# Optimization experiments

Hardware: AMD Instinct MI355X
Metric: run time of the kernel (lower is better)

The kernel has to match this reference:

```python
import jax, jax.numpy as jnp
import numpy as np

FP16_HUGE = 2.0 ** 15
NUM_HEAD = 4
LN_EPS = 1e-5


def setup_inputs() -> dict:
    key = jax.random.key(0)
    ks = jax.random.split(key, 12)
    B, N, D = 1, 256, 128
    H = NUM_HEAD
    inp = {
        "pair_act": jax.random.normal(ks[0], (B, N, N, D), dtype=jnp.float32),
        "pair_mask": jnp.ones((B, N, N), dtype=jnp.float32),
        "ln_scale": jnp.ones((D,), dtype=jnp.float32),
        "ln_bias": jnp.zeros((D,), dtype=jnp.float32),
        # torch Linear weight layout: [out_dim, in_dim]; applied as x @ W.T
        "w2d": jax.random.normal(ks[1], (H, D), dtype=jnp.float32) / np.sqrt(D),
        "wq": jax.random.normal(ks[2], (D, D), dtype=jnp.float32) / np.sqrt(D),
        "wk": jax.random.normal(ks[3], (D, D), dtype=jnp.float32) / np.sqrt(D),
        "wv": jax.random.normal(ks[4], (D, D), dtype=jnp.float32) / np.sqrt(D),
        "wg": jax.random.normal(ks[5], (D, D), dtype=jnp.float32) / np.sqrt(D),
        "bg": jnp.ones((D,), dtype=jnp.float32),  # gating bias init = 1.0
        "wo": jax.random.normal(ks[6], (D, D), dtype=jnp.float32) * 0.02,
        "bo": jnp.zeros((D,), dtype=jnp.float32),
    }
    return inp


def reference(pair_act, pair_mask, ln_scale, ln_bias, w2d, wq, wk, wv, wg, bg, wo, bo):
    B, N, _, D = pair_act.shape
    H = NUM_HEAD
    kd = D // H  # per-head key/value dim
    scale = kd ** (-0.5)

    # mask bias: [B, N(row), 1, 1, N(key)]
    bias = (FP16_HUGE * (pair_mask - 1.0))[:, :, None, None, :]

    # LayerNorm (fp32, eps=1e-5)
    mu = jnp.mean(pair_act, axis=-1, keepdims=True)
    var = jnp.mean(jnp.square(pair_act - mu), axis=-1, keepdims=True)
    x = (pair_act - mu) * jax.lax.rsqrt(var + LN_EPS) * ln_scale + ln_bias

    # non-batched per-head bias: [B, 1, H, N, N]
    nb = jnp.einsum("bijd,hd->bhij", x, w2d)[:, None]

    q = (x @ wq.T).reshape(B, N, N, H, kd) * scale  # [B, r, i, H, kd]
    k = (x @ wk.T).reshape(B, N, N, H, kd)
    v = (x @ wv.T).reshape(B, N, N, H, kd)

    logits = jnp.einsum("brihk,brjhk->brhij", q, k) + bias + nb  # [B, r, H, i, j]
    w = jax.nn.softmax(logits, axis=-1)
    o = jnp.einsum("brhij,brjhv->brihv", w, v)  # [B, r, i, H, kd]

    g = jax.nn.sigmoid(x @ wg.T + bg).reshape(B, N, N, H, kd)
    o = (o * g).reshape(B, N, N, D)

    out = o @ wo.T + bo
    return out * pair_mask[..., None]
```

## Files before the change

### kernel.cpp

```cpp
#include <hip/hip_runtime.h>
#include <hip/hip_bf16.h>

typedef unsigned short u16;
typedef __attribute__((ext_vector_type(8))) short bf16x8;
typedef __attribute__((ext_vector_type(4))) float f32x4;
typedef __attribute__((address_space(3))) unsigned lds_u32;
typedef const __attribute__((address_space(1))) unsigned glb_u32;

#define N 256
#define D 128
#define NH 4
#define KD 32
#define NN 65536
#define QK_SCALE 0.17677669529663687f
#define LOG2E 1.4426950408889634f
#define HUGE_MASK 32768.0f

__device__ __forceinline__ float b2f(u16 s) {
  union { float f; unsigned u; } x; x.u = ((unsigned)s) << 16; return x.f;
}
__device__ __forceinline__ u16 f2b(float f) {
  union { float f; unsigned u; } x; x.f = f;
  unsigned r = x.u + 0x7fff + ((x.u >> 16) & 1);
  return (u16)(r >> 16);
}
__device__ __forceinline__ float exp2v(float x) {
  float r; __asm__("v_exp_f32 %0, %1" : "=v"(r) : "v"(x)); return r;
}

__global__ __launch_bounds__(256) void prep_w_kernel(
    const float* __restrict__ wq, const float* __restrict__ wk,
    const float* __restrict__ wv, const float* __restrict__ wg,
    const float* __restrict__ wo, u16* __restrict__ wb)
{
  int idx = blockIdx.x * 256 + threadIdx.x;
  const float* srcs[5] = {wq, wk, wv, wg, wo};
  int mat = idx >> 11, rem = idx & 2047;
  int row = rem >> 4, g = rem & 15;
  int gp = (g + (row & 15)) & 15;
  const float* s = srcs[mat] + row * 128 + g * 8;
  float4 f0 = *(const float4*)(s);
  float4 f1 = *(const float4*)(s + 4);
  uint4 pk;
  pk.x = (unsigned)f2b(f0.x) | ((unsigned)f2b(f0.y) << 16);
  pk.y = (unsigned)f2b(f0.z) | ((unsigned)f2b(f0.w) << 16);
  pk.z = (unsigned)f2b(f1.x) | ((unsigned)f2b(f1.y) << 16);
  pk.w = (unsigned)f2b(f1.z) | ((unsigned)f2b(f1.w) << 16);
  *(uint4*)(wb + (size_t)mat * 16384 + row * 128 + gp * 8) = pk;
}

template <int NW>
__device__ __forceinline__ void async_stage(const u16* __restrict__ gsrc, u16* lds, int tid) {
  int lane = tid & 63, wave = tid >> 6;
#pragma unroll
  for (int p = 0; p < 32 / NW; p++) {
    int c = wave * (32 / NW) + p;
    __builtin_amdgcn_global_load_lds((glb_u32*)(gsrc + c * 512 + lane * 8),
                                     (lds_u32*)(lds + c * 512), 16, 0, 0);
  }
}

__global__ __launch_bounds__(512) void projln_kernel(
    const float* __restrict__ pa, const float* __restrict__ lns, const float* __restrict__ lnb,
    const float* __restrict__ w2d, const u16* __restrict__ wb, const float* __restrict__ bg,
    u16* __restrict__ q, u16* __restrict__ k, u16* __restrict__ v, u16* __restrict__ g,
    float* __restrict__ nb)
{
  __shared__ __align__(16) u16 Wl[2][16384];
  int tid = threadIdx.x;
  int wave = tid >> 6, lane = tid & 63;
  int lr = lane & 15, quad = lane >> 4;

  async_stage<8>(wb, Wl[0], tid);

  bf16x8 a[4];
  int row = blockIdx.x * 128 + wave * 16 + lr;
  {
    const float* rp = pa + (size_t)row * D;
    float xv[4][8];
    float s = 0.f, ss = 0.f;
#pragma unroll
    for (int ks = 0; ks < 4; ks++) {
      float4 a0 = *(const float4*)(rp + ks * 32 + quad * 8);
      float4 a1 = *(const float4*)(rp + ks * 32 + quad * 8 + 4);
      xv[ks][0] = a0.x; xv[ks][1] = a0.y; xv[ks][2] = a0.z; xv[ks][3] = a0.w;
      xv[ks][4] = a1.x; xv[ks][5] = a1.y; xv[ks][6] = a1.z; xv[ks][7] = a1.w;
#pragma unroll
      for (int j = 0; j < 8; j++) { s += xv[ks][j]; ss += xv[ks][j] * xv[ks][j]; }
    }
    s  += __shfl_xor(s, 16, 64);  ss += __shfl_xor(ss, 16, 64);
    s  += __shfl_xor(s, 32, 64);  ss += __shfl_xor(ss, 32, 64);
    float mu = s * (1.0f / D);
    float var = ss * (1.0f / D) - mu * mu;
    float rs = rsqrtf(var + 1e-5f);
#pragma unroll
    for (int ks = 0; ks < 4; ks++) {
      float4 s0 = *(const float4*)(lns + ks * 32 + quad * 8);
      float4 s1 = *(const float4*)(lns + ks * 32 + quad * 8 + 4);
      float4 b0 = *(const float4*)(lnb + ks * 32 + quad * 8);
      float4 b1 = *(const float4*)(lnb + ks * 32 + quad * 8 + 4);
      float sc[8] = {s0.x,s0.y,s0.z,s0.w,s1.x,s1.y,s1.z,s1.w};
      float bi[8] = {b0.x,b0.y,b0.z,b0.w,b1.x,b1.y,b1.z,b1.w};
#pragma unroll
      for (int j = 0; j < 8; j++) xv[ks][j] = (xv[ks][j] - mu) * rs * sc[j] + bi[j];
    }
#pragma unroll
    for (int h = 0; h < NH; h++) {
      float p = 0.f;
#pragma unroll
      for (int ks = 0; ks < 4; ks++) {
        float4 w0 = *(const float4*)(w2d + h * D + ks * 32 + quad * 8);
        float4 w1 = *(const float4*)(w2d + h * D + ks * 32 + quad * 8 + 4);
        p += xv[ks][0]*w0.x + xv[ks][1]*w0.y + xv[ks][2]*w0.z + xv[ks][3]*w0.w
           + xv[ks][4]*w1.x + xv[ks][5]*w1.y + xv[ks][6]*w1.z + xv[ks][7]*w1.w;
      }
      p += __shfl_xor(p, 16, 64);
      p += __shfl_xor(p, 32, 64);
      if (quad == 0)
        nb[(size_t)h * NN + row] = p * LOG2E;
    }
#pragma unroll
    for (int ks = 0; ks < 4; ks++)
#pragma unroll
      for (int j = 0; j < 8; j++) a[ks][j] = (short)f2b(xv[ks][j]);
  }
  __syncthreads();

  u16* Os[4] = {q, k, v, g};
#pragma unroll
  for (int mat = 0; mat < 4; mat++) {
    if (mat < 3) async_stage<8>(wb + (size_t)(mat + 1) * 16384, Wl[(mat + 1) & 1], tid);
    const u16* Wcur = Wl[mat & 1];
    f32x4 acc[2][4];
#pragma unroll
    for (int tg = 0; tg < 2; tg++)
#pragma unroll
      for (int e = 0; e < 4; e++) acc[tg][e] = (f32x4){0.f, 0.f, 0.f, 0.f};
#pragma unroll
    for (int ks = 0; ks < 4; ks++) {
#pragma unroll
      for (int tg = 0; tg < 2; tg++) {
#pragma unroll
        for (int e = 0; e < 4; e++) {
          int nrow = tg * 64 + 4 * lr + e;
          int gp = (ks * 4 + quad + (nrow & 15)) & 15;
          bf16x8 b = *(const bf16x8*)(&Wcur[nrow * 128 + gp * 8]);
          acc[tg][e] = __builtin_amdgcn_mfma_f32_16x16x32_bf16(a[ks], b, acc[tg][e], 0, 0, 0);
        }
      }
    }
    u16* O = Os[mat];
    int row0 = blockIdx.x * 128 + wave * 16 + quad * 4;
#pragma unroll
    for (int tg = 0; tg < 2; tg++) {
      int c0 = tg * 64 + 4 * lr;
      float bg0 = 0.f, bg1 = 0.f, bg2 = 0.f, bg3 = 0.f;
      if (mat == 3) { bg0 = bg[c0]; bg1 = bg[c0+1]; bg2 = bg[c0+2]; bg3 = bg[c0+3]; }
#pragma unroll
      for (int reg = 0; reg < 4; reg++) {
        float v0 = acc[tg][0][reg], v1 = acc[tg][1][reg];
        float v2 = acc[tg][2][reg], v3 = acc[tg][3][reg];
        if (mat == 0) {
          v0 *= QK_SCALE * LOG2E; v1 *= QK_SCALE * LOG2E;
          v2 *= QK_SCALE * LOG2E; v3 *= QK_SCALE * LOG2E;
        }
        if (mat == 3) {
          v0 = 1.0f / (1.0f + __expf(-(v0 + bg0)));
          v1 = 1.0f / (1.0f + __expf(-(v1 + bg1)));
          v2 = 1.0f / (1.0f + __expf(-(v2 + bg2)));
          v3 = 1.0f / (1.0f + __expf(-(v3 + bg3)));
        }
        uint2 pk;
        pk.x = (unsigned)f2b(v0) | ((unsigned)f2b(v1) << 16);
        pk.y = (unsigned)f2b(v2) | ((unsigned)f2b(v3) << 16);
        *(uint2*)(O + (size_t)(row0 + reg) * D + c0) = pk;
      }
    }
    __syncthreads();
  }
}

__global__ __launch_bounds__(512) void attn_kernel(
    const u16* __restrict__ q, const u16* __restrict__ k, const u16* __restrict__ v,
    const u16* __restrict__ g, const float* __restrict__ nb, const float* __restrict__ mask,
    u16* __restrict__ og)
{
  __shared__ __align__(16) u16 Kf[8192];
  __shared__ __align__(16) u16 Vf[8192];
  __shared__ float bias_lds[256];
  int h = blockIdx.x & 3, r = blockIdx.x >> 2;
  int tid = threadIdx.x;
  {
    int j = tid & 255;
    if (tid < 256) {
      const u16* krow = k + ((size_t)r * N + j) * D + h * KD;
      int t = j >> 4, lrj = j & 15;
#pragma unroll
      for (int qc = 0; qc < 4; qc++)
        *(bf16x8*)(&Kf[((t * 4 + qc) * 16 + lrj) * 8]) = *(const bf16x8*)(krow + qc * 8);
      bias_lds[j] = (HUGE_MASK * LOG2E) * (mask[r * N + j] - 1.0f);
    }
    const u16* vrow = v + ((size_t)r * N + j) * D + h * KD;
    int ksrc = j >> 5, jrel = j & 31;
    int qv, jv;
    if (jrel < 16) { qv = jrel >> 2; jv = jrel & 3; }
    else           { qv = (jrel & 15) >> 2; jv = 4 + (jrel & 3); }
    int chalf = (tid >> 8) * 16;
#pragma unroll
    for (int cc = 0; cc < 16; cc++) {
      int c = chalf + cc;
      Vf[(((ksrc * 2 + (c & 1)) * 4 + qv) * 16 + (c >> 1)) * 8 + jv] = vrow[c];
    }
  }
  __syncthreads();
  int wave = tid >> 6, lane = tid & 63;
  int lr = lane & 15, quad = lane >> 4;
  const float* nbh = nb + (size_t)h * NN;

  for (int pp = 0; pp < 2; pp++) {
    int i0 = pp * 128 + wave * 16;
    int irow = i0 + lr;
    bf16x8 af = *(const bf16x8*)(q + ((size_t)r * N + irow) * D + h * KD + quad * 8);
    const float* nbrow = nbh + (size_t)irow * N;
    float m = 0.f, ls = 0.f;
    f32x4 oa = (f32x4){0.f,0.f,0.f,0.f}, ob = (f32x4){0.f,0.f,0.f,0.f};
#pragma unroll 1
    for (int c = 0; c < 2; c++) {
      f32x4 S[8];
#pragma unroll
      for (int tt = 0; tt < 8; tt++) {
        int t = c * 8 + tt;
        int jb = t * 16 + quad * 4;
        float4 nb4 = *(const float4*)(nbrow + jb);
        float4 b4  = *(const float4*)(&bias_lds[jb]);
        f32x4 ci;
        ci[0] = nb4.x + b4.x; ci[1] = nb4.y + b4.y;
        ci[2] = nb4.z + b4.z; ci[3] = nb4.w + b4.w;
        bf16x8 kfr = *(const bf16x8*)(&Kf[((t * 4 + quad) * 16 + lr) * 8]);
        S[tt] = __builtin_amdgcn_mfma_f32_16x16x32_bf16(kfr, af, ci, 0, 0, 0);
      }
      float m0 = -3e38f, m1 = -3e38f, m2 = -3e38f, m3 = -3e38f;
#pragma unroll
      for (int tt = 0; tt < 8; tt++) {
        m0 = fmaxf(m0, S[tt][0]); m1 = fmaxf(m1, S[tt][1]);
        m2 = fmaxf(m2, S[tt][2]); m3 = fmaxf(m3, S[tt][3]);
      }
      float ma = fmaxf(fmaxf(m0, m1), fmaxf(m2, m3));
      ma = fmaxf(ma, __shfl_xor(ma, 16, 64));
      ma = fmaxf(ma, __shfl_xor(ma, 32, 64));
      if (c == 0) {
        m = ma;
      } else {
        float mnew = fmaxf(m, ma);
        float sc = exp2v(m - mnew);
        m = mnew;
        ls *= sc;
        float s0 = __shfl(sc, quad * 4 + 0, 64);
        float s1 = __shfl(sc, quad * 4 + 1, 64);
        float s2 = __shfl(sc, quad * 4 + 2, 64);
        float s3 = __shfl(sc, quad * 4 + 3, 64);
        oa[0] *= s0; oa[1] *= s1; oa[2] *= s2; oa[3] *= s3;
        ob[0] *= s0; ob[1] *= s1; ob[2] *= s2; ob[3] *= s3;
      }
#pragma unroll
      for (int kk = 0; kk < 4; kk++) {
        int ks = c * 4 + kk;
        float p0 = exp2v(S[2*kk][0] - m);
        float p1 = exp2v(S[2*kk][1] - m);
        float p2 = exp2v(S[2*kk][2] - m);
        float p3 = exp2v(S[2*kk][3] - m);
        float p4 = exp2v(S[2*kk+1][0] - m);
        float p5 = exp2v(S[2*kk+1][1] - m);
        float p6 = exp2v(S[2*kk+1][2] - m);
        float p7 = exp2v(S[2*kk+1][3] - m);
        ls += ((p0 + p1) + (p2 + p3)) + ((p4 + p5) + (p6 + p7));
        union { bf16x8 v; unsigned u[4]; } pa;
        __asm__("v_cvt_pk_bf16_f32 %0, %1, %2" : "=v"(pa.u[0]) : "v"(p0), "v"(p1));
        __asm__("v_cvt_pk_bf16_f32 %0, %1, %2" : "=v"(pa.u[1]) : "v"(p2), "v"(p3));
        __asm__("v_cvt_pk_bf16_f32 %0, %1, %2" : "=v"(pa.u[2]) : "v"(p4), "v"(p5));
        __asm__("v_cvt_pk_bf16_f32 %0, %1, %2" : "=v"(pa.u[3]) : "v"(p6), "v"(p7));
        bf16x8 vb0 = *(const bf16x8*)(&Vf[(((ks * 2 + 0) * 4 + quad) * 16 + lr) * 8]);
        oa = __builtin_amdgcn_mfma_f32_16x16x32_bf16(pa.v, vb0, oa, 0, 0, 0);
        bf16x8 vb1 = *(const bf16x8*)(&Vf[(((ks * 2 + 1) * 4 + quad) * 16 + lr) * 8]);
        ob = __builtin_amdgcn_mfma_f32_16x16x32_bf16(pa.v, vb1, ob, 0, 0, 0);
      }
    }
    float lsum = ls;
    lsum += __shfl_xor(lsum, 16, 64);
    lsum += __shfl_xor(lsum, 32, 64);
    float invd = __builtin_amdgcn_rcpf(lsum);

#pragma unroll
    for (int reg = 0; reg < 4; reg++) {
      float inv = __shfl(invd, quad * 4 + reg, 64);
      int i = i0 + quad * 4 + reg;
      size_t base = ((size_t)r * N + i) * D + h * KD + 2 * lr;
      unsigned gv = *(const unsigned*)(g + base);
      float r0 = oa[reg] * inv * b2f((u16)(gv & 0xffff));
      float r1 = ob[reg] * inv * b2f((u16)(gv >> 16));
      *(unsigned*)(og + base) = (unsigned)f2b(r0) | ((unsigned)f2b(r1) << 16);
    }
  }
}

__global__ __launch_bounds__(512) void out_kernel(
    const u16* __restrict__ og, const u16* __restrict__ wob, const float* __restrict__ bo,
    const float* __restrict__ mask, float* __restrict__ out)
{
  __shared__ __align__(16) u16 Wlds[16384];
  int tid = threadIdx.x;
  async_stage<8>(wob, Wlds, tid);
  int wave = tid >> 6, lane = tid & 63;
  int lr = lane & 15, quad = lane >> 4;
  bf16x8 a[4];
  int arow = blockIdx.x * 128 + wave * 16 + lr;
#pragma unroll
  for (int ks = 0; ks < 4; ks++)
    a[ks] = *(const bf16x8*)(og + (size_t)arow * D + ks * 32 + quad * 8);
  __syncthreads();
  f32x4 acc[2][4];
#pragma unroll
  for (int tg = 0; tg < 2; tg++)
#pragma unroll
    for (int e = 0; e < 4; e++) acc[tg][e] = (f32x4){0.f, 0.f, 0.f, 0.f};
#pragma unroll
  for (int ks = 0; ks < 4; ks++) {
#pragma unroll
    for (int tg = 0; tg < 2; tg++) {
#pragma unroll
      for (int e = 0; e < 4; e++) {
        int nrow = tg * 64 + 4 * lr + e;
        int gp = (ks * 4 + quad + (nrow & 15)) & 15;
        bf16x8 b = *(const bf16x8*)(&Wlds[nrow * 128 + gp * 8]);
        acc[tg][e] = __builtin_amdgcn_mfma_f32_16x16x32_bf16(a[ks], b, acc[tg][e], 0, 0, 0);
      }
    }
  }
  int row0 = blockIdx.x * 128 + wave * 16 + quad * 4;
#pragma unroll
  for (int tg = 0; tg < 2; tg++) {
    int c0 = tg * 64 + 4 * lr;
    float4 bo4 = *(const float4*)(bo + c0);
#pragma unroll
    for (int reg = 0; reg < 4; reg++) {
      int pos = row0 + reg;
      float mk = mask[pos];
      float4 o4;
      o4.x = (acc[tg][0][reg] + bo4.x) * mk;
      o4.y = (acc[tg][1][reg] + bo4.y) * mk;
      o4.z = (acc[tg][2][reg] + bo4.z) * mk;
      o4.w = (acc[tg][3][reg] + bo4.w) * mk;
      *(float4*)(out + (size_t)pos * D + c0) = o4;
    }
  }
}

extern "C" void kernel_launch(void* const* d_in, const int* in_sizes, int n_in,
                              void* d_out, int out_size, void* d_ws, size_t ws_size,
                              hipStream_t stream)
{
  const float* pa   = (const float*)d_in[0];
  const float* mask = (const float*)d_in[1];
  const float* lns  = (const float*)d_in[2];
  const float* lnb  = (const float*)d_in[3];
  const float* w2d  = (const float*)d_in[4];
  const float* wq   = (const float*)d_in[5];
  const float* wk   = (const float*)d_in[6];
  const float* wv   = (const float*)d_in[7];
  const float* wg   = (const float*)d_in[8];
  const float* bg   = (const float*)d_in[9];
  const float* wo   = (const float*)d_in[10];
  const float* bo   = (const float*)d_in[11];

  const size_t ARR = (size_t)NN * D;
  u16* q  = (u16*)d_ws;
  u16* k  = q + ARR;
  u16* v  = k + ARR;
  u16* g  = v + ARR;
  u16* og = g + ARR;
  float* nb = (float*)(og + ARR);
  u16* wb = (u16*)(nb + (size_t)NH * NN);

  prep_w_kernel<<<40, 256, 0, stream>>>(wq, wk, wv, wg, wo, wb);
  projln_kernel<<<512, 512, 0, stream>>>(pa, lns, lnb, w2d, wb, bg, q, k, v, g, nb);
  attn_kernel<<<N * NH, 512, 0, stream>>>(q, k, v, g, nb, mask, og);
  out_kernel<<<512, 512, 0, stream>>>(og, wb + 4 * 16384, bo, mask, (float*)d_out);
}
```

Baseline: 186.6 us.

## Fuse attention and output projection into one kernel with per-block head loop

Merges attn_kernel and out_kernel so each block handles half the query rows of one pair row and loops over all four heads. The gated attention output is written to LDS in a swizzled layout instead of global memory, then multiplied by the staged Wo to produce the final output. This removes the og global round trip and one kernel launch. In exchange, K/V for every head are restaged serially with extra syncs, K/V are loaded twice per row (once per half), and the grid shrinks from 1024 to 512 blocks, giving less parallelism.

```diff
diff --git a/kernel.cpp b/kernel.cpp
--- a/kernel.cpp
+++ b/kernel.cpp
@@ -180,48 +180,51 @@
   }
 }
 
-__global__ __launch_bounds__(512) void attn_kernel(
+__global__ __launch_bounds__(512) void attn_out_kernel(
     const u16* __restrict__ q, const u16* __restrict__ k, const u16* __restrict__ v,
     const u16* __restrict__ g, const float* __restrict__ nb, const float* __restrict__ mask,
-    u16* __restrict__ og)
+    const u16* __restrict__ wob, const float* __restrict__ bo, float* __restrict__ out)
 {
-  __shared__ __align__(16) u16 Kf[8192];
-  __shared__ __align__(16) u16 Vf[8192];
+  __shared__ __align__(16) u16 KV[16384];
+  __shared__ __align__(16) u16 og_lds[16384];
   __shared__ float bias_lds[256];
-  int h = blockIdx.x & 3, r = blockIdx.x >> 2;
+  int r = blockIdx.x >> 1, half = blockIdx.x & 1;
   int tid = threadIdx.x;
-  {
-    int j = tid & 255;
-    if (tid < 256) {
-      const u16* krow = k + ((size_t)r * N + j) * D + h * KD;
-      int t = j >> 4, lrj = j & 15;
-#pragma unroll
-      for (int qc = 0; qc < 4; qc++)
-        *(bf16x8*)(&Kf[((t * 4 + qc) * 16 + lrj) * 8]) = *(const bf16x8*)(krow + qc * 8);
-      bias_lds[j] = (HUGE_MASK * LOG2E) * (mask[r * N + j] - 1.0f);
-    }
-    const u16* vrow = v + ((size_t)r * N + j) * D + h * KD;
-    int ksrc = j >> 5, jrel = j & 31;
-    int qv, jv;
-    if (jrel < 16) { qv = jrel >> 2; jv = jrel & 3; }
-    else           { qv = (jrel & 15) >> 2; jv = 4 + (jrel & 3); }
-    int chalf = (tid >> 8) * 16;
+  int wave = tid >> 6, lane = tid & 63;
+  int lr = lane & 15, quad = lane >> 4;
+
+  if (tid < 256) bias_lds[tid] = (HUGE_MASK * LOG2E) * (mask[r * N + tid] - 1.0f);
+
+  int irow = half * 128 + wave * 16 + lr;
+  const u16* qbase = q + ((size_t)r * N + irow) * D + quad * 8;
+  bf16x8 af[NH];
+#pragma unroll
+  for (int h = 0; h < NH; h++) af[h] = *(const bf16x8*)(qbase + h * KD);
+
+  int kj = tid >> 1, kc = tid & 1;
+  int tK = kj >> 4, lrK = kj & 15;
+  int vj = tid & 255;
+  int jrel = vj & 31, ksrc = vj >> 5;
+  int qv = (jrel & 15) >> 2;
+  int jv = (jrel & 3) | ((jrel >> 4) << 2);
+  int chalf = (tid >> 8) * 16;
+
+#pragma unroll 1
+  for (int h = 0; h < NH; h++) {
+    const u16* krow = k + ((size_t)r * N + kj) * D + h * KD + kc * 16;
+    bf16x8 k0 = *(const bf16x8*)(krow);
+    bf16x8 k1 = *(const bf16x8*)(krow + 8);
+    *(bf16x8*)(&KV[((tK * 4 + kc * 2 + 0) * 16 + lrK) * 8]) = k0;
+    *(bf16x8*)(&KV[((tK * 4 + kc * 2 + 1) * 16 + lrK) * 8]) = k1;
+    const u16* vrow = v + ((size_t)r * N + vj) * D + h * KD;
 #pragma unroll
     for (int cc = 0; cc < 16; cc++) {
       int c = chalf + cc;
-      Vf[(((ksrc * 2 + (c & 1)) * 4 + qv) * 16 + (c >> 1)) * 8 + jv] = vrow[c];
-    }
-  }
-  __syncthreads();
-  int wave = tid >> 6, lane = tid & 63;
-  int lr = lane & 15, quad = lane >> 4;
-  const float* nbh = nb + (size_t)h * NN;
-
-  for (int pp = 0; pp < 2; pp++) {
-    int i0 = pp * 128 + wave * 16;
-    int irow = i0 + lr;
-    bf16x8 af = *(const bf16x8*)(q + ((size_t)r * N + irow) * D + h * KD + quad * 8);
-    const float* nbrow = nbh + (size_t)irow * N;
+      KV[8192 + (((ksrc * 2 + (c & 1)) * 4 + qv) * 16 + (c >> 1)) * 8 + jv] = vrow[c];
+    }
+    __syncthreads();
+
+    const float* nbrow = nb + (size_t)h * NN + (size_t)irow * N;
     float m = 0.f, ls = 0.f;
     f32x4 oa = (f32x4){0.f,0.f,0.f,0.f}, ob = (f32x4){0.f,0.f,0.f,0.f};
 #pragma unroll 1
@@ -236,8 +239,8 @@
         f32x4 ci;
         ci[0] = nb4.x + b4.x; ci[1] = nb4.y + b4.y;
         ci[2] = nb4.z + b4.z; ci[3] = nb4.w + b4.w;
-        bf16x8 kfr = *(const bf16x8*)(&Kf[((t * 4 + quad) * 16 + lr) * 8]);
-        S[tt] = __builtin_amdgcn_mfma_f32_16x16x32_bf16(kfr, af, ci, 0, 0, 0);
+        bf16x8 kfr = *(const bf16x8*)(&KV[((t * 4 + quad) * 16 + lr) * 8]);
+        S[tt] = __builtin_amdgcn_mfma_f32_16x16x32_bf16(kfr, af[h], ci, 0, 0, 0);
       }
       float m0 = -3e38f, m1 = -3e38f, m2 = -3e38f, m3 = -3e38f;
 #pragma unroll
@@ -279,9 +282,9 @@
         __asm__("v_cvt_pk_bf16_f32 %0, %1, %2" : "=v"(pa.u[1]) : "v"(p2), "v"(p3));
         __asm__("v_cvt_pk_bf16_f32 %0, %1, %2" : "=v"(pa.u[2]) : "v"(p4), "v"(p5));
         __asm__("v_cvt_pk_bf16_f32 %0, %1, %2" : "=v"(pa.u[3]) : "v"(p6), "v"(p7));
-        bf16x8 vb0 = *(const bf16x8*)(&Vf[(((ks * 2 + 0) * 4 + quad) * 16 + lr) * 8]);
+        bf16x8 vb0 = *(const bf16x8*)(&KV[8192 + (((ks * 2 + 0) * 4 + quad) * 16 + lr) * 8]);
         oa = __builtin_amdgcn_mfma_f32_16x16x32_bf16(pa.v, vb0, oa, 0, 0, 0);
-        bf16x8 vb1 = *(const bf16x8*)(&Vf[(((ks * 2 + 1) * 4 + quad) * 16 + lr) * 8]);
+        bf16x8 vb1 = *(const bf16x8*)(&KV[8192 + (((ks * 2 + 1) * 4 + quad) * 16 + lr) * 8]);
         ob = __builtin_amdgcn_mfma_f32_16x16x32_bf16(pa.v, vb1, ob, 0, 0, 0);
       }
     }
@@ -293,31 +296,29 @@
 #pragma unroll
     for (int reg = 0; reg < 4; reg++) {
       float inv = __shfl(invd, quad * 4 + reg, 64);
-      int i = i0 + quad * 4 + reg;
-      size_t base = ((size_t)r * N + i) * D + h * KD + 2 * lr;
-      unsigned gv = *(const unsigned*)(g + base);
+      int l = wave * 16 + quad * 4 + reg;
+      size_t gb = ((size_t)r * N + half * 128 + l) * D + h * KD + 2 * lr;
+      unsigned gv = *(const unsigned*)(g + gb);
       float r0 = oa[reg] * inv * b2f((u16)(gv & 0xffff));
       float r1 = ob[reg] * inv * b2f((u16)(gv >> 16));
-      *(unsigned*)(og + base) = (unsigned)f2b(r0) | ((unsigned)f2b(r1) << 16);
-    }
-  }
-}
-
-__global__ __launch_bounds__(512) void out_kernel(
-    const u16* __restrict__ og, const u16* __restrict__ wob, const float* __restrict__ bo,
-    const float* __restrict__ mask, float* __restrict__ out)
-{
-  __shared__ __align__(16) u16 Wlds[16384];
-  int tid = threadIdx.x;
-  async_stage<8>(wob, Wlds, tid);
-  int wave = tid >> 6, lane = tid & 63;
-  int lr = lane & 15, quad = lane >> 4;
+      int col = h * KD + 2 * lr;
+      int gp = ((col >> 3) + l) & 15;
+      *(unsigned*)(&og_lds[l * 128 + gp * 8 + (col & 7)]) =
+          (unsigned)f2b(r0) | ((unsigned)f2b(r1) << 16);
+    }
+    __syncthreads();
+  }
+
+  async_stage<8>(wob, KV, tid);
+  __syncthreads();
+
   bf16x8 a[4];
-  int arow = blockIdx.x * 128 + wave * 16 + lr;
-#pragma unroll
-  for (int ks = 0; ks < 4; ks++)
-    a[ks] = *(const bf16x8*)(og + (size_t)arow * D + ks * 32 + quad * 8);
-  __syncthreads();
+  int l = wave * 16 + lr;
+#pragma unroll
+  for (int ks = 0; ks < 4; ks++) {
+    int gp = (ks * 4 + quad + (l & 15)) & 15;
+    a[ks] = *(const bf16x8*)(&og_lds[l * 128 + gp * 8]);
+  }
   f32x4 acc[2][4];
 #pragma unroll
   for (int tg = 0; tg < 2; tg++)
@@ -331,19 +332,19 @@
       for (int e = 0; e < 4; e++) {
         int nrow = tg * 64 + 4 * lr + e;
         int gp = (ks * 4 + quad + (nrow & 15)) & 15;
-        bf16x8 b = *(const bf16x8*)(&Wlds[nrow * 128 + gp * 8]);
+        bf16x8 b = *(const bf16x8*)(&KV[nrow * 128 + gp * 8]);
         acc[tg][e] = __builtin_amdgcn_mfma_f32_16x16x32_bf16(a[ks], b, acc[tg][e], 0, 0, 0);
       }
     }
   }
-  int row0 = blockIdx.x * 128 + wave * 16 + quad * 4;
+  int flat0 = r * N + half * 128 + wave * 16 + quad * 4;
 #pragma unroll
   for (int tg = 0; tg < 2; tg++) {
     int c0 = tg * 64 + 4 * lr;
     float4 bo4 = *(const float4*)(bo + c0);
 #pragma unroll
     for (int reg = 0; reg < 4; reg++) {
-      int pos = row0 + reg;
+      int pos = flat0 + reg;
       float mk = mask[pos];
       float4 o4;
       o4.x = (acc[tg][0][reg] + bo4.x) * mk;
@@ -377,12 +378,11 @@
   u16* k  = q + ARR;
   u16* v  = k + ARR;
   u16* g  = v + ARR;
-  u16* og = g + ARR;
-  float* nb = (float*)(og + ARR);
+  float* nb = (float*)(g + ARR);
   u16* wb = (u16*)(nb + (size_t)NH * NN);
 
   prep_w_kernel<<<40, 256, 0, stream>>>(wq, wk, wv, wg, wo, wb);
   projln_kernel<<<512, 512, 0, stream>>>(pa, lns, lnb, w2d, wb, bg, q, k, v, g, nb);
-  attn_kernel<<<N * NH, 512, 0, stream>>>(q, k, v, g, nb, mask, og);
-  out_kernel<<<512, 512, 0, stream>>>(og, wb + 4 * 16384, bo, mask, (float*)d_out);
-}
+  attn_out_kernel<<<512, 512, 0, stream>>>(q, k, v, g, nb, mask, wb + 4 * 16384, bo,
+                                           (float*)d_out);
+}
```

After: 225.5 us. 20.9% more time.

## Write K and V in attention fragment layout from projection kernel

Applied to the files above, without the earlier changes.

The projection kernel now writes K and V straight into the per-(row, head) fragment layouts that the attention kernel uses in LDS. Attention then stages K/V with linear async global-to-LDS copies instead of a scattered gather and transpose. This removes the scalar, uncoalesced V transpose from the attention prologue. In exchange, the projection epilogue does scattered 2-byte V stores and strided K stores.

```diff
diff --git a/kernel.cpp b/kernel.cpp
--- a/kernel.cpp
+++ b/kernel.cpp
@@ -49,12 +49,12 @@
   *(uint4*)(wb + (size_t)mat * 16384 + row * 128 + gp * 8) = pk;
 }
 
-template <int NW>
-__device__ __forceinline__ void async_stage(const u16* __restrict__ gsrc, u16* lds, int tid) {
+template <int CPW>
+__device__ __forceinline__ void stage_lin(const u16* __restrict__ gsrc, u16* lds, int tid) {
   int lane = tid & 63, wave = tid >> 6;
 #pragma unroll
-  for (int p = 0; p < 32 / NW; p++) {
-    int c = wave * (32 / NW) + p;
+  for (int p = 0; p < CPW; p++) {
+    int c = wave * CPW + p;
     __builtin_amdgcn_global_load_lds((glb_u32*)(gsrc + c * 512 + lane * 8),
                                      (lds_u32*)(lds + c * 512), 16, 0, 0);
   }
@@ -63,7 +63,7 @@
 __global__ __launch_bounds__(512) void projln_kernel(
     const float* __restrict__ pa, const float* __restrict__ lns, const float* __restrict__ lnb,
     const float* __restrict__ w2d, const u16* __restrict__ wb, const float* __restrict__ bg,
-    u16* __restrict__ q, u16* __restrict__ k, u16* __restrict__ v, u16* __restrict__ g,
+    u16* __restrict__ q, u16* __restrict__ kf, u16* __restrict__ vf, u16* __restrict__ g,
     float* __restrict__ nb)
 {
   __shared__ __align__(16) u16 Wl[2][16384];
@@ -71,7 +71,7 @@
   int wave = tid >> 6, lane = tid & 63;
   int lr = lane & 15, quad = lane >> 4;
 
-  async_stage<8>(wb, Wl[0], tid);
+  stage_lin<4>(wb, Wl[0], tid);
 
   bf16x8 a[4];
   int row = blockIdx.x * 128 + wave * 16 + lr;
@@ -126,10 +126,9 @@
   }
   __syncthreads();
 
-  u16* Os[4] = {q, k, v, g};
 #pragma unroll
   for (int mat = 0; mat < 4; mat++) {
-    if (mat < 3) async_stage<8>(wb + (size_t)(mat + 1) * 16384, Wl[(mat + 1) & 1], tid);
+    if (mat < 3) stage_lin<4>(wb + (size_t)(mat + 1) * 16384, Wl[(mat + 1) & 1], tid);
     const u16* Wcur = Wl[mat & 1];
     f32x4 acc[2][4];
 #pragma unroll
@@ -149,7 +148,6 @@
         }
       }
     }
-    u16* O = Os[mat];
     int row0 = blockIdx.x * 128 + wave * 16 + quad * 4;
 #pragma unroll
     for (int tg = 0; tg < 2; tg++) {
@@ -170,10 +168,36 @@
           v2 = 1.0f / (1.0f + __expf(-(v2 + bg2)));
           v3 = 1.0f / (1.0f + __expf(-(v3 + bg3)));
         }
-        uint2 pk;
-        pk.x = (unsigned)f2b(v0) | ((unsigned)f2b(v1) << 16);
-        pk.y = (unsigned)f2b(v2) | ((unsigned)f2b(v3) << 16);
-        *(uint2*)(O + (size_t)(row0 + reg) * D + c0) = pk;
+        int R = row0 + reg;
+        if (mat == 1) {
+          int rr = R >> 8, j = R & 255;
+          int t = j >> 4, lrj = j & 15;
+          int h2 = c0 >> 5, cc = c0 & 31, qc = cc >> 3, s2 = cc & 7;
+          uint2 pk;
+          pk.x = (unsigned)f2b(v0) | ((unsigned)f2b(v1) << 16);
+          pk.y = (unsigned)f2b(v2) | ((unsigned)f2b(v3) << 16);
+          *(uint2*)(kf + (size_t)(rr * NH + h2) * 8192 +
+                    ((t * 4 + qc) * 16 + lrj) * 8 + s2) = pk;
+        } else if (mat == 2) {
+          int rr = R >> 8, j = R & 255;
+          int ks2 = j >> 5, jrel = j & 31;
+          int qv = (jrel & 15) >> 2;
+          int jv = (jrel & 3) | ((jrel >> 4) << 2);
+          int h2 = c0 >> 5, cc = c0 & 31;
+          size_t base = (size_t)(rr * NH + h2) * 8192;
+          u16 vs[4] = {f2b(v0), f2b(v1), f2b(v2), f2b(v3)};
+#pragma unroll
+          for (int i2 = 0; i2 < 4; i2++) {
+            int c = cc + i2, e = c & 1, l = c >> 1;
+            vf[base + (((ks2 * 2 + e) * 4 + qv) * 16 + l) * 8 + jv] = vs[i2];
+          }
+        } else {
+          u16* O = (mat == 0) ? q : g;
+          uint2 pk;
+          pk.x = (unsigned)f2b(v0) | ((unsigned)f2b(v1) << 16);
+          pk.y = (unsigned)f2b(v2) | ((unsigned)f2b(v3) << 16);
+          *(uint2*)(O + (size_t)R * D + c0) = pk;
+        }
       }
     }
     __syncthreads();
@@ -181,7 +205,7 @@
 }
 
 __global__ __launch_bounds__(512) void attn_kernel(
-    const u16* __restrict__ q, const u16* __restrict__ k, const u16* __restrict__ v,
+    const u16* __restrict__ q, const u16* __restrict__ kf, const u16* __restrict__ vf,
     const u16* __restrict__ g, const float* __restrict__ nb, const float* __restrict__ mask,
     u16* __restrict__ og)
 {
@@ -190,29 +214,11 @@
   __shared__ float bias_lds[256];
   int h = blockIdx.x & 3, r = blockIdx.x >> 2;
   int tid = threadIdx.x;
-  {
-    int j = tid & 255;
-    if (tid < 256) {
-      const u16* krow = k + ((size_t)r * N + j) * D + h * KD;
-      int t = j >> 4, lrj = j & 15;
-#pragma unroll
-      for (int qc = 0; qc < 4; qc++)
-        *(bf16x8*)(&Kf[((t * 4 + qc) * 16 + lrj) * 8]) = *(const bf16x8*)(krow + qc * 8);
-      bias_lds[j] = (HUGE_MASK * LOG2E) * (mask[r * N + j] - 1.0f);
-    }
-    const u16* vrow = v + ((size_t)r * N + j) * D + h * KD;
-    int ksrc = j >> 5, jrel = j & 31;
-    int qv, jv;
-    if (jrel < 16) { qv = jrel >> 2; jv = jrel & 3; }
-    else           { qv = (jrel & 15) >> 2; jv = 4 + (jrel & 3); }
-    int chalf = (tid >> 8) * 16;
-#pragma unroll
-    for (int cc = 0; cc < 16; cc++) {
-      int c = chalf + cc;
-      Vf[(((ksrc * 2 + (c & 1)) * 4 + qv) * 16 + (c >> 1)) * 8 + jv] = vrow[c];
-    }
-  }
+  stage_lin<2>(kf + (size_t)(r * NH + h) * 8192, Kf, tid);
+  stage_lin<2>(vf + (size_t)(r * NH + h) * 8192, Vf, tid);
+  if (tid < 256) bias_lds[tid] = (HUGE_MASK * LOG2E) * (mask[r * N + tid] - 1.0f);
   __syncthreads();
+
   int wave = tid >> 6, lane = tid & 63;
   int lr = lane & 15, quad = lane >> 4;
   const float* nbh = nb + (size_t)h * NN;
@@ -309,7 +315,7 @@
 {
   __shared__ __align__(16) u16 Wlds[16384];
   int tid = threadIdx.x;
-  async_stage<8>(wob, Wlds, tid);
+  stage_lin<4>(wob, Wlds, tid);
   int wave = tid >> 6, lane = tid & 63;
   int lr = lane & 15, quad = lane >> 4;
   bf16x8 a[4];
@@ -374,15 +380,15 @@
 
   const size_t ARR = (size_t)NN * D;
   u16* q  = (u16*)d_ws;
-  u16* k  = q + ARR;
-  u16* v  = k + ARR;
-  u16* g  = v + ARR;
+  u16* kf = q + ARR;
+  u16* vf = kf + ARR;
+  u16* g  = vf + ARR;
   u16* og = g + ARR;
   float* nb = (float*)(og + ARR);
   u16* wb = (u16*)(nb + (size_t)NH * NN);
 
   prep_w_kernel<<<40, 256, 0, stream>>>(wq, wk, wv, wg, wo, wb);
-  projln_kernel<<<512, 512, 0, stream>>>(pa, lns, lnb, w2d, wb, bg, q, k, v, g, nb);
-  attn_kernel<<<N * NH, 512, 0, stream>>>(q, k, v, g, nb, mask, og);
+  projln_kernel<<<512, 512, 0, stream>>>(pa, lns, lnb, w2d, wb, bg, q, kf, vf, g, nb);
+  attn_kernel<<<N * NH, 512, 0, stream>>>(q, kf, vf, g, nb, mask, og);
   out_kernel<<<512, 512, 0, stream>>>(og, wb + 4 * 16384, bo, mask, (float*)d_out);
 }
```

Result: no change. 187.6 us (+0.5%).
